# Performance work log

Hardware: AMD Instinct MI355X
Metric: run time of the kernel (lower is better)

## Reference

```python
import jax, jax.numpy as jnp
import numpy as np

D_MODEL = 1024
N_HEADS = 16
D_HEAD = D_MODEL // N_HEADS
LN_EPS = 1e-5


def setup_inputs() -> dict:
    key = jax.random.key(0)
    ks = jax.random.split(key, 6)
    s = 1.0 / np.sqrt(D_MODEL)
    x = jax.random.normal(ks[0], (4, 2048, D_MODEL), dtype=jnp.float32)
    w_qkv = jax.random.uniform(ks[1], (3 * D_MODEL, D_MODEL), jnp.float32, -s, s)
    w_out = jax.random.uniform(ks[2], (D_MODEL, D_MODEL), jnp.float32, -s, s)
    w_ffn1 = jax.random.uniform(ks[3], (2 * D_MODEL, D_MODEL), jnp.float32, -s, s)
    w_ffn2 = jax.random.uniform(ks[4], (D_MODEL, 2 * D_MODEL), jnp.float32, -1.0 / np.sqrt(2 * D_MODEL), 1.0 / np.sqrt(2 * D_MODEL))
    return {
        "x": x,
        "w_qkv": w_qkv,
        "w_out": w_out,
        "w_ffn1": w_ffn1,
        "w_ffn2": w_ffn2,
        "g1": jnp.ones((D_MODEL,), jnp.float32),
        "b1": jnp.zeros((D_MODEL,), jnp.float32),
        "g2": jnp.ones((D_MODEL,), jnp.float32),
        "b2": jnp.zeros((D_MODEL,), jnp.float32),
        "temperature": jnp.float32(0.05),
    }


def _layernorm(x, g, b):
    mu = jnp.mean(x, axis=-1, keepdims=True)
    var = jnp.mean(jnp.square(x - mu), axis=-1, keepdims=True)
    return (x - mu) * jax.lax.rsqrt(var + LN_EPS) * g + b


def _l2norm(x, eps=1e-12):
    # matches F.normalize(p=2, dim=-1)
    n = jnp.sqrt(jnp.sum(jnp.square(x), axis=-1, keepdims=True))
    return x / jnp.maximum(n, eps)


def reference(x, w_qkv, w_out, w_ffn1, w_ffn2, g1, b1, g2, b2, temperature):
    B, N, C = x.shape
    residual = x
    h = _layernorm(x, g1, b1)
    qkv = h @ w_qkv.T  # [B,N,3C]
    qkv = qkv.reshape(B, N, 3, N_HEADS, D_HEAD).transpose(2, 0, 3, 1, 4)
    q, k, v = qkv[0], qkv[1], qkv[2]  # each [B,H,N,d]
    qn = _l2norm(q)
    kn = _l2norm(k)
    attn = jnp.einsum('bhnd,bhmd->bhnm', qn, kn) / temperature
    attn = jax.nn.softmax(attn, axis=-1)
    out = jnp.einsum('bhnm,bhmd->bhnd', attn, v)  # [B,H,N,d]
    out = out.transpose(0, 2, 1, 3).reshape(B, N, C)
    x = residual + out @ w_out.T
    residual = x
    h = _layernorm(x, g2, b2)
    h = jax.nn.relu(h @ w_ffn1.T) @ w_ffn2.T
    return residual + h
```

## Files before the change

### kernel.cpp

```cpp
#include <hip/hip_runtime.h>
#include <cstdint>
#include <cstddef>
#include <math.h>

typedef __attribute__((ext_vector_type(8))) short short8;
typedef __attribute__((ext_vector_type(4))) float f32x4;

#define D_MODEL 1024
#define NHEADS 16
#define DHEAD 64
#define BATCH 4
#define SEQ 2048
#define MTOK (BATCH * SEQ)

__device__ __forceinline__ unsigned short f2bf(float f) {
  union { float f; unsigned u; } v; v.f = f;
  unsigned r = v.u + 0x7fffu + ((v.u >> 16) & 1u);
  return (unsigned short)(r >> 16);
}
__device__ __forceinline__ float bf2f(unsigned short u) {
  union { unsigned u; float f; } v; v.u = ((unsigned)u) << 16;
  return v.f;
}
__device__ __forceinline__ unsigned cvt_pk_bf16(float a, float b) {
  unsigned u;
  asm("v_cvt_pk_bf16_f32 %0, %1, %2" : "=v"(u) : "v"(a), "v"(b));
  return u;
}

typedef const __attribute__((address_space(1))) unsigned int* gas1_t;
typedef __attribute__((address_space(3))) unsigned int* las3_t;
__device__ __forceinline__ void gload16(const unsigned short* g, unsigned short* l) {
  __builtin_amdgcn_global_load_lds((gas1_t)g, (las3_t)l, 16, 0, 0);
}

#define MFMA_BF16(a, b, c) __builtin_amdgcn_mfma_f32_16x16x32_bf16(a, b, c, 0, 0, 0)

__global__ __launch_bounds__(256) void f32_to_bf16_all(const float* __restrict__ s0,
                                                       const float* __restrict__ s1,
                                                       const float* __restrict__ s2,
                                                       const float* __restrict__ s3,
                                                       unsigned short* __restrict__ d0,
                                                       unsigned short* __restrict__ d1,
                                                       unsigned short* __restrict__ d2,
                                                       unsigned short* __restrict__ d3) {
  int j = blockIdx.x * 256 + threadIdx.x;
  const float* s;
  unsigned short* d;
  if (j < 786432) { s = s0; d = d0; }
  else if ((j -= 786432) < 262144) { s = s1; d = d1; }
  else if ((j -= 262144) < 524288) { s = s2; d = d2; }
  else { j -= 524288; s = s3; d = d3; }
  float4 v = ((const float4*)s)[j];
  ushort4 o;
  o.x = f2bf(v.x); o.y = f2bf(v.y); o.z = f2bf(v.z); o.w = f2bf(v.w);
  ((ushort4*)d)[j] = o;
}

__global__ __launch_bounds__(256) void ln_fwd(const float* __restrict__ x, const float* __restrict__ g,
                                              const float* __restrict__ b,
                                              unsigned short* __restrict__ out) {
  const int row = blockIdx.x, t = threadIdx.x;
  float4 v = *(const float4*)(x + (size_t)row * D_MODEL + t * 4);
  float s = v.x + v.y + v.z + v.w;
  float s2 = v.x * v.x + v.y * v.y + v.z * v.z + v.w * v.w;
#pragma unroll
  for (int m = 1; m < 64; m <<= 1) { s += __shfl_xor(s, m); s2 += __shfl_xor(s2, m); }
  __shared__ float red[8];
  int wv = t >> 6;
  if ((t & 63) == 0) { red[wv] = s; red[4 + wv] = s2; }
  __syncthreads();
  s = red[0] + red[1] + red[2] + red[3];
  s2 = red[4] + red[5] + red[6] + red[7];
  float mu = s * (1.f / D_MODEL);
  float var = s2 * (1.f / D_MODEL) - mu * mu;
  float rs = rsqrtf(var + 1e-5f);
  float4 gg = *(const float4*)(g + t * 4);
  float4 bb = *(const float4*)(b + t * 4);
  ushort4 o;
  o.x = f2bf((v.x - mu) * rs * gg.x + bb.x);
  o.y = f2bf((v.y - mu) * rs * gg.y + bb.y);
  o.z = f2bf((v.z - mu) * rs * gg.z + bb.z);
  o.w = f2bf((v.w - mu) * rs * gg.w + bb.w);
  *(ushort4*)(out + (size_t)row * D_MODEL + t * 4) = o;
}

template <int EPI>
__global__ __launch_bounds__(256) void gemm_bt2(const unsigned short* __restrict__ A,
                                                const unsigned short* __restrict__ B,
                                                const float* __restrict__ R,
                                                const float* __restrict__ Tptr,
                                                void* __restrict__ Cout, int M, int N, int K) {
  constexpr int BM = 128, BN = 128, BK = 32;
  __shared__ unsigned short lA[2][BM * BK], lB[2][BN * BK];
  const int tid = threadIdx.x, lane = tid & 63, wave = tid >> 6;
  const int lo = lane & 15, g = lane >> 4;
  const int nbx = gridDim.x;
  const int o = blockIdx.y * nbx + blockIdx.x;
  const int cpx = (nbx * gridDim.y) >> 3;
  const int w = (o & 7) * cpx + (o >> 3);
  const int bx = w % nbx, by = w / nbx;
  const int bm = by * BM, bn = bx * BN;
  const int wr = wave >> 1, wc = wave & 1;
  f32x4 acc[4][4] = {};
  const int c0 = wave * 128 + lane, c1 = c0 + 64;
  const unsigned short* gA0 = A + (size_t)(bm + (c0 >> 2)) * K + (c0 & 3) * 8;
  const unsigned short* gA1 = A + (size_t)(bm + (c1 >> 2)) * K + (c1 & 3) * 8;
  const unsigned short* gB0 = B + (size_t)(bn + (c0 >> 2)) * K + (c0 & 3) * 8;
  const unsigned short* gB1 = B + (size_t)(bn + (c1 >> 2)) * K + (c1 & 3) * 8;
  const int nk = K / BK;
  auto stage = [&](int buf, int kt) {
    const size_t ko = (size_t)kt * BK;
    gload16(gA0 + ko, &lA[buf][(wave * 128) * 8]);
    gload16(gA1 + ko, &lA[buf][(wave * 128 + 64) * 8]);
    gload16(gB0 + ko, &lB[buf][(wave * 128) * 8]);
    gload16(gB1 + ko, &lB[buf][(wave * 128 + 64) * 8]);
  };
  stage(0, 0);
  for (int kt = 0; kt < nk; ++kt) {
    __syncthreads();
    if (kt + 1 < nk) stage((kt + 1) & 1, kt + 1);
    const unsigned short* La = &lA[kt & 1][0];
    const unsigned short* Lb = &lB[kt & 1][0];
    short8 af[4], bfr[4];
#pragma unroll
    for (int m = 0; m < 4; ++m)
      af[m] = *(const short8*)(La + (wr * 64 + m * 16 + lo) * BK + g * 8);
#pragma unroll
    for (int n = 0; n < 4; ++n)
      bfr[n] = *(const short8*)(Lb + (wc * 64 + n * 16 + lo) * BK + g * 8);
#pragma unroll
    for (int m = 0; m < 4; ++m)
#pragma unroll
      for (int n = 0; n < 4; ++n) acc[m][n] = MFMA_BF16(af[m], bfr[n], acc[m][n]);
  }
  const int r0 = bm + wr * 64 + g * 4;
  const int c0c = bn + wc * 64 + lo;
  if (EPI == 3) {
    const int hb = bn + wc * 64;
    const bool isq = hb < 1024, isk = (hb >= 1024) && (hb < 2048);
    const float qs = 1.44269504088896f / Tptr[0];
#pragma unroll
    for (int m = 0; m < 4; ++m)
#pragma unroll
      for (int r = 0; r < 4; ++r) {
        float sc = 1.0f;
        if (isq || isk) {
          float ss = 0.f;
#pragma unroll
          for (int n = 0; n < 4; ++n) ss += acc[m][n][r] * acc[m][n][r];
          ss += __shfl_xor(ss, 1);
          ss += __shfl_xor(ss, 2);
          ss += __shfl_xor(ss, 4);
          ss += __shfl_xor(ss, 8);
          sc = 1.0f / fmaxf(sqrtf(ss), 1e-12f);
          if (isq) sc *= qs;
        }
#pragma unroll
        for (int n = 0; n < 4; ++n) {
          size_t off = (size_t)(r0 + m * 16 + r) * N + (c0c + n * 16);
          ((unsigned short*)Cout)[off] = f2bf(acc[m][n][r] * sc);
        }
      }
  } else {
#pragma unroll
    for (int m = 0; m < 4; ++m)
#pragma unroll
      for (int n = 0; n < 4; ++n) {
#pragma unroll
        for (int r = 0; r < 4; ++r) {
          size_t off = (size_t)(r0 + m * 16 + r) * N + (c0c + n * 16);
          float v = acc[m][n][r];
          if (EPI == 0) ((unsigned short*)Cout)[off] = f2bf(v);
          else if (EPI == 1) ((float*)Cout)[off] = R[off] + v;
          else ((unsigned short*)Cout)[off] = f2bf(fmaxf(v, 0.f));
        }
      }
  }
}

__global__ __launch_bounds__(256) void transpose_v(const unsigned short* __restrict__ qkv,
                                                   unsigned short* __restrict__ vt) {
  __shared__ unsigned short tile[64][80];
  const int blk = blockIdx.x;
  const int ntile = blk & 31, h = (blk >> 5) & 15, b = blk >> 9;
  const int t = threadIdx.x;
  const int tt = t >> 2, c4 = t & 3;
  size_t rowbase = (size_t)(b * SEQ + ntile * 64 + tt) * 3072 + h * 64 + c4 * 16;
  const unsigned short* pv = qkv + rowbase + 2048;
  *(short8*)&tile[tt][c4 * 16] = *(const short8*)pv;
  *(short8*)&tile[tt][c4 * 16 + 8] = *(const short8*)(pv + 8);
  __syncthreads();
  const int d = tt;
  short8 o0, o1;
#pragma unroll
  for (int j = 0; j < 8; ++j) o0[j] = (short)tile[c4 * 16 + j][d];
#pragma unroll
  for (int j = 0; j < 8; ++j) o1[j] = (short)tile[c4 * 16 + 8 + j][d];
  size_t vr = (size_t)((b * NHEADS + h) * DHEAD + d) * SEQ + ntile * 64 + c4 * 16;
  *(short8*)(vt + vr) = o0;
  *(short8*)(vt + vr + 8) = o1;
}

__global__ __launch_bounds__(512) void attn_fwd7(const unsigned short* __restrict__ qkv,
                                                 const unsigned short* __restrict__ vt,
                                                 unsigned short* __restrict__ out,
                                                 const float* __restrict__ temp) {
  constexpr int LDT = 72;
  constexpr int LDP = 66;
  __shared__ unsigned short lK[2][64 * LDT];
  __shared__ unsigned short lV[2][64 * LDT];
  __shared__ unsigned short pP[16][16 * LDP];
  const int d_ = blockIdx.x;
  const int bh = d_ & 63, qt = d_ >> 6;
  const int b = bh >> 4, h = bh & 15;
  const int tid = threadIdx.x, lane = tid & 63, wave = tid >> 6;
  const int lo = lane & 15, g = lane >> 4;
  const int qr0 = qt * 256 + wave * 32;
  const float M0 = 1.05f * 1.44269504088896f / temp[0];
  const f32x4 minit = {-M0, -M0, -M0, -M0};
  const unsigned short* qrowA = qkv + (size_t)(b * SEQ + qr0 + lo) * 3072 + h * 64 + g * 8;
  const unsigned short* qrowB = qrowA + (size_t)16 * 3072;
  const short8 qA0 = *(const short8*)qrowA;
  const short8 qA1 = *(const short8*)(qrowA + 32);
  const short8 qB0 = *(const short8*)qrowB;
  const short8 qB1 = *(const short8*)(qrowB + 32);
  const int srow = tid >> 3, scol = (tid & 7) * 8;
  const unsigned short* gK = qkv + (size_t)(b * SEQ + srow) * 3072 + 1024 + h * 64 + scol;
  const unsigned short* gV = vt + ((size_t)((b * NHEADS + h) * DHEAD) + srow) * SEQ + scol;
  short8 rk = *(const short8*)gK;
  short8 rv = *(const short8*)gV;
  *(short8*)&lK[0][srow * LDT + scol] = rk;
  *(short8*)&lV[0][srow * LDT + scol] = rv;
  f32x4 oA[4] = {}, oB[4] = {};
  float lA_ = 0.f, lB_ = 0.f;
  unsigned short* PbA = &pP[wave][0];
  unsigned short* PbB = &pP[8 + wave][0];
  constexpr int NT = SEQ / 64;
  for (int t = 0; t < NT; ++t) {
    __syncthreads();
    const unsigned short* Kb = &lK[t & 1][0];
    const unsigned short* Vb = &lV[t & 1][0];
    if (t + 1 < NT) {
      rk = *(const short8*)(gK + (size_t)(t + 1) * 64 * 3072);
      rv = *(const short8*)(gV + (t + 1) * 64);
    }
    f32x4 sA[4], sB[4];
    __builtin_amdgcn_s_setprio(1);
#pragma unroll
    for (int jt = 0; jt < 4; ++jt) {
      short8 kf0 = *(const short8*)(Kb + (jt * 16 + lo) * LDT + g * 8);
      short8 kf1 = *(const short8*)(Kb + (jt * 16 + lo) * LDT + 32 + g * 8);
      sA[jt] = MFMA_BF16(kf1, qA1, MFMA_BF16(kf0, qA0, minit));
      sB[jt] = MFMA_BF16(kf1, qB1, MFMA_BF16(kf0, qB0, minit));
    }
    __builtin_amdgcn_s_setprio(0);
    float psA = 0.f, psB = 0.f;
#pragma unroll
    for (int jt = 0; jt < 4; ++jt) {
      float a0 = exp2f(sA[jt][0]), a1 = exp2f(sA[jt][1]);
      float a2 = exp2f(sA[jt][2]), a3 = exp2f(sA[jt][3]);
      sA[jt][0] = a0; sA[jt][1] = a1; sA[jt][2] = a2; sA[jt][3] = a3;
      psA += (a0 + a1) + (a2 + a3);
      float b0 = exp2f(sB[jt][0]), b1 = exp2f(sB[jt][1]);
      float b2 = exp2f(sB[jt][2]), b3 = exp2f(sB[jt][3]);
      sB[jt][0] = b0; sB[jt][1] = b1; sB[jt][2] = b2; sB[jt][3] = b3;
      psB += (b0 + b1) + (b2 + b3);
    }
    lA_ += psA;
    lB_ += psB;
#pragma unroll
    for (int jt = 0; jt < 4; ++jt) {
      *(unsigned*)(PbA + lo * LDP + jt * 16 + g * 4) = cvt_pk_bf16(sA[jt][0], sA[jt][1]);
      *(unsigned*)(PbA + lo * LDP + jt * 16 + g * 4 + 2) = cvt_pk_bf16(sA[jt][2], sA[jt][3]);
      *(unsigned*)(PbB + lo * LDP + jt * 16 + g * 4) = cvt_pk_bf16(sB[jt][0], sB[jt][1]);
      *(unsigned*)(PbB + lo * LDP + jt * 16 + g * 4 + 2) = cvt_pk_bf16(sB[jt][2], sB[jt][3]);
    }
    short8 pA0 = *(const short8*)(PbA + lo * LDP + g * 8);
    short8 pA1 = *(const short8*)(PbA + lo * LDP + 32 + g * 8);
    short8 pB0 = *(const short8*)(PbB + lo * LDP + g * 8);
    short8 pB1 = *(const short8*)(PbB + lo * LDP + 32 + g * 8);
    __builtin_amdgcn_s_setprio(1);
#pragma unroll
    for (int c = 0; c < 4; ++c) {
      short8 vb0 = *(const short8*)(Vb + (c * 16 + lo) * LDT + g * 8);
      short8 vb1 = *(const short8*)(Vb + (c * 16 + lo) * LDT + 32 + g * 8);
      oA[c] = MFMA_BF16(vb1, pA1, MFMA_BF16(vb0, pA0, oA[c]));
      oB[c] = MFMA_BF16(vb1, pB1, MFMA_BF16(vb0, pB0, oB[c]));
    }
    __builtin_amdgcn_s_setprio(0);
    if (t + 1 < NT) {
      *(short8*)&lK[(t + 1) & 1][srow * LDT + scol] = rk;
      *(short8*)&lV[(t + 1) & 1][srow * LDT + scol] = rv;
    }
  }
  lA_ += __shfl_xor(lA_, 16);
  lA_ += __shfl_xor(lA_, 32);
  lB_ += __shfl_xor(lB_, 16);
  lB_ += __shfl_xor(lB_, 32);
  const float rA = 1.0f / lA_, rB = 1.0f / lB_;
  unsigned short* orowA = out + (size_t)(b * SEQ + qr0 + lo) * D_MODEL + h * 64 + g * 4;
  unsigned short* orowB = orowA + (size_t)16 * D_MODEL;
#pragma unroll
  for (int c = 0; c < 4; ++c)
#pragma unroll
    for (int r = 0; r < 4; r += 2) {
      *(unsigned*)(orowA + c * 16 + r) = cvt_pk_bf16(oA[c][r] * rA, oA[c][r + 1] * rA);
      *(unsigned*)(orowB + c * 16 + r) = cvt_pk_bf16(oB[c][r] * rB, oB[c][r + 1] * rB);
    }
}

extern "C" void kernel_launch(void* const* d_in, const int* in_sizes, int n_in, void* d_out,
                              int out_size, void* d_ws, size_t ws_size, hipStream_t stream) {
  const float* x = (const float*)d_in[0];
  const float* w_qkv = (const float*)d_in[1];
  const float* w_out = (const float*)d_in[2];
  const float* w_ffn1 = (const float*)d_in[3];
  const float* w_ffn2 = (const float*)d_in[4];
  const float* g1 = (const float*)d_in[5];
  const float* b1 = (const float*)d_in[6];
  const float* g2 = (const float*)d_in[7];
  const float* b2 = (const float*)d_in[8];
  const float* temp = (const float*)d_in[9];
  float* outp = (float*)d_out;

  char* ws = (char*)d_ws;
  size_t off = 0;
  auto alloc = [&](size_t bytes) {
    void* p = ws + off;
    off += (bytes + 255) & ~(size_t)255;
    return p;
  };
  unsigned short* wqkv_bf = (unsigned short*)alloc((size_t)3072 * 1024 * 2);
  unsigned short* wout_bf = (unsigned short*)alloc((size_t)1024 * 1024 * 2);
  unsigned short* wf1_bf = (unsigned short*)alloc((size_t)2048 * 1024 * 2);
  unsigned short* wf2_bf = (unsigned short*)alloc((size_t)1024 * 2048 * 2);
  unsigned short* h_bf = (unsigned short*)alloc((size_t)MTOK * 1024 * 2);
  unsigned short* qkv_bf = (unsigned short*)alloc((size_t)MTOK * 3072 * 2);
  unsigned short* vt_bf = (unsigned short*)alloc((size_t)BATCH * NHEADS * DHEAD * SEQ * 2);
  unsigned short* ao_bf = (unsigned short*)alloc((size_t)MTOK * 1024 * 2);
  float* x2 = (float*)alloc((size_t)MTOK * 1024 * 4);

  f32_to_bf16_all<<<8192, 256, 0, stream>>>(w_qkv, w_out, w_ffn1, w_ffn2, wqkv_bf, wout_bf, wf1_bf,
                                            wf2_bf);
  ln_fwd<<<MTOK, 256, 0, stream>>>(x, g1, b1, h_bf);
  gemm_bt2<3><<<dim3(3072 / 128, MTOK / 128), 256, 0, stream>>>(h_bf, wqkv_bf, nullptr, temp,
                                                                (void*)qkv_bf, MTOK, 3072, 1024);
  transpose_v<<<BATCH * NHEADS * (SEQ / 64), 256, 0, stream>>>(qkv_bf, vt_bf);
  attn_fwd7<<<BATCH * NHEADS * (SEQ / 256), 512, 0, stream>>>(qkv_bf, vt_bf, ao_bf, temp);
  gemm_bt2<1><<<dim3(1024 / 128, MTOK / 128), 256, 0, stream>>>(ao_bf, wout_bf, x, nullptr,
                                                                (void*)x2, MTOK, 1024, 1024);
  ln_fwd<<<MTOK, 256, 0, stream>>>(x2, g2, b2, h_bf);
  gemm_bt2<2><<<dim3(2048 / 128, MTOK / 128), 256, 0, stream>>>(h_bf, wf1_bf, nullptr, nullptr,
                                                                (void*)qkv_bf, MTOK, 2048, 1024);
  gemm_bt2<1><<<dim3(1024 / 128, MTOK / 128), 256, 0, stream>>>(qkv_bf, wf2_bf, x2, nullptr,
                                                                (void*)outp, MTOK, 1024, 2048);
}
```

Baseline: 367.8 us.

## Rewrite attention with 32x32 MFMA, register P via permlane swap, swizzled LDS

Replaces the 16x16x32 MFMA attention kernel with one built on 32x32x16 MFMA. The softmax probabilities are reshuffled in registers with permlane32_swap, so the LDS round-trip for P goes away. K/V tiles now use an XOR-swizzled unpadded LDS layout instead of padded rows, and blocks shrink to 4 waves covering 128 query rows, which doubles the grid. The aims are fewer LDS accesses and bank conflicts plus denser matrix instructions. The cost is more register pressure and a different occupancy balance.

Result: faster. 347.2 us (-5.6%).

```diff
diff --git a/kernel.cpp b/kernel.cpp
--- a/kernel.cpp
+++ b/kernel.cpp
@@ -5,6 +5,8 @@
 
 typedef __attribute__((ext_vector_type(8))) short short8;
 typedef __attribute__((ext_vector_type(4))) float f32x4;
+typedef __attribute__((ext_vector_type(16))) float f32x16;
+typedef __attribute__((ext_vector_type(2))) unsigned uint2v;
 
 #define D_MODEL 1024
 #define NHEADS 16
@@ -35,6 +37,7 @@
 }
 
 #define MFMA_BF16(a, b, c) __builtin_amdgcn_mfma_f32_16x16x32_bf16(a, b, c, 0, 0, 0)
+#define MFMA32(a, b, c) __builtin_amdgcn_mfma_f32_32x32x16_bf16(a, b, c, 0, 0, 0)
 
 __global__ __launch_bounds__(256) void f32_to_bf16_all(const float* __restrict__ s0,
                                                        const float* __restrict__ s1,
@@ -202,111 +205,113 @@
   *(short8*)(vt + vr + 8) = o1;
 }
 
-__global__ __launch_bounds__(512) void attn_fwd7(const unsigned short* __restrict__ qkv,
+__global__ __launch_bounds__(256) void attn_fwd8(const unsigned short* __restrict__ qkv,
                                                  const unsigned short* __restrict__ vt,
                                                  unsigned short* __restrict__ out,
                                                  const float* __restrict__ temp) {
-  constexpr int LDT = 72;
-  constexpr int LDP = 66;
-  __shared__ unsigned short lK[2][64 * LDT];
-  __shared__ unsigned short lV[2][64 * LDT];
-  __shared__ unsigned short pP[16][16 * LDP];
-  const int d_ = blockIdx.x;
-  const int bh = d_ & 63, qt = d_ >> 6;
+  __shared__ unsigned short lK[2][64 * 64];
+  __shared__ unsigned short lV[2][64 * 64];
+  const int blk = blockIdx.x;
+  const int bh = blk & 63, qt = blk >> 6;
   const int b = bh >> 4, h = bh & 15;
   const int tid = threadIdx.x, lane = tid & 63, wave = tid >> 6;
-  const int lo = lane & 15, g = lane >> 4;
-  const int qr0 = qt * 256 + wave * 32;
+  const int l5 = lane >> 5, l31 = lane & 31;
+  const int qr0 = qt * 128 + wave * 32;
   const float M0 = 1.05f * 1.44269504088896f / temp[0];
-  const f32x4 minit = {-M0, -M0, -M0, -M0};
-  const unsigned short* qrowA = qkv + (size_t)(b * SEQ + qr0 + lo) * 3072 + h * 64 + g * 8;
-  const unsigned short* qrowB = qrowA + (size_t)16 * 3072;
-  const short8 qA0 = *(const short8*)qrowA;
-  const short8 qA1 = *(const short8*)(qrowA + 32);
-  const short8 qB0 = *(const short8*)qrowB;
-  const short8 qB1 = *(const short8*)(qrowB + 32);
-  const int srow = tid >> 3, scol = (tid & 7) * 8;
-  const unsigned short* gK = qkv + (size_t)(b * SEQ + srow) * 3072 + 1024 + h * 64 + scol;
-  const unsigned short* gV = vt + ((size_t)((b * NHEADS + h) * DHEAD) + srow) * SEQ + scol;
-  short8 rk = *(const short8*)gK;
-  short8 rv = *(const short8*)gV;
-  *(short8*)&lK[0][srow * LDT + scol] = rk;
-  *(short8*)&lV[0][srow * LDT + scol] = rv;
-  f32x4 oA[4] = {}, oB[4] = {};
-  float lA_ = 0.f, lB_ = 0.f;
-  unsigned short* PbA = &pP[wave][0];
-  unsigned short* PbB = &pP[8 + wave][0];
+  f32x16 minit;
+#pragma unroll
+  for (int r = 0; r < 16; ++r) minit[r] = -M0;
+  const unsigned short* qrow = qkv + (size_t)(b * SEQ + qr0 + l31) * 3072 + h * 64 + l5 * 8;
+  short8 qf[4];
+#pragma unroll
+  for (int t = 0; t < 4; ++t) qf[t] = *(const short8*)(qrow + t * 16);
+  const int srow = tid >> 3, slot = tid & 7;
+  const int sw0 = ((slot ^ (srow & 7)) * 8);
+  const unsigned short* gK = qkv + (size_t)(b * SEQ + srow) * 3072 + 1024 + h * 64 + slot * 8;
+  const unsigned short* gV = vt + ((size_t)(bh * 64) + srow) * SEQ + slot * 8;
+  short8 rk0 = *(const short8*)gK;
+  short8 rk1 = *(const short8*)(gK + (size_t)32 * 3072);
+  short8 rv0 = *(const short8*)gV;
+  short8 rv1 = *(const short8*)(gV + (size_t)32 * SEQ);
+  *(short8*)&lK[0][srow * 64 + sw0] = rk0;
+  *(short8*)&lK[0][(srow + 32) * 64 + sw0] = rk1;
+  *(short8*)&lV[0][srow * 64 + sw0] = rv0;
+  *(short8*)&lV[0][(srow + 32) * 64 + sw0] = rv1;
+  f32x16 o0 = {}, o1 = {};
+  float lsum = 0.f;
   constexpr int NT = SEQ / 64;
   for (int t = 0; t < NT; ++t) {
     __syncthreads();
     const unsigned short* Kb = &lK[t & 1][0];
     const unsigned short* Vb = &lV[t & 1][0];
     if (t + 1 < NT) {
-      rk = *(const short8*)(gK + (size_t)(t + 1) * 64 * 3072);
-      rv = *(const short8*)(gV + (t + 1) * 64);
+      rk0 = *(const short8*)(gK + (size_t)(t + 1) * 64 * 3072);
+      rk1 = *(const short8*)(gK + (size_t)((t + 1) * 64 + 32) * 3072);
+      rv0 = *(const short8*)(gV + (t + 1) * 64);
+      rv1 = *(const short8*)(gV + (size_t)32 * SEQ + (t + 1) * 64);
     }
-    f32x4 sA[4], sB[4];
-    __builtin_amdgcn_s_setprio(1);
-#pragma unroll
-    for (int jt = 0; jt < 4; ++jt) {
-      short8 kf0 = *(const short8*)(Kb + (jt * 16 + lo) * LDT + g * 8);
-      short8 kf1 = *(const short8*)(Kb + (jt * 16 + lo) * LDT + 32 + g * 8);
-      sA[jt] = MFMA_BF16(kf1, qA1, MFMA_BF16(kf0, qA0, minit));
-      sB[jt] = MFMA_BF16(kf1, qB1, MFMA_BF16(kf0, qB0, minit));
+#pragma unroll
+    for (int tile = 0; tile < 2; ++tile) {
+      f32x16 s = minit;
+      __builtin_amdgcn_s_setprio(1);
+#pragma unroll
+      for (int td = 0; td < 4; ++td) {
+        const int row = tile * 32 + l31;
+        const int sl = ((2 * td + l5) ^ (row & 7)) * 8;
+        short8 kf = *(const short8*)(Kb + row * 64 + sl);
+        s = MFMA32(kf, qf[td], s);
+      }
+      __builtin_amdgcn_s_setprio(0);
+      float p[16];
+      float ps = 0.f;
+#pragma unroll
+      for (int r = 0; r < 16; ++r) { p[r] = exp2f(s[r]); ps += p[r]; }
+      lsum += ps;
+      unsigned a0 = cvt_pk_bf16(p[0], p[1]), a1 = cvt_pk_bf16(p[2], p[3]);
+      unsigned a2 = cvt_pk_bf16(p[4], p[5]), a3 = cvt_pk_bf16(p[6], p[7]);
+      unsigned c0 = cvt_pk_bf16(p[8], p[9]), c1 = cvt_pk_bf16(p[10], p[11]);
+      unsigned c2 = cvt_pk_bf16(p[12], p[13]), c3 = cvt_pk_bf16(p[14], p[15]);
+      uint2v w0 = __builtin_amdgcn_permlane32_swap(a0, a2, false, false);
+      uint2v w1 = __builtin_amdgcn_permlane32_swap(a1, a3, false, false);
+      uint2v w2 = __builtin_amdgcn_permlane32_swap(c0, c2, false, false);
+      uint2v w3 = __builtin_amdgcn_permlane32_swap(c1, c3, false, false);
+      union { unsigned u[4]; short8 v; } f0, f1;
+      f0.u[0] = w0.x; f0.u[1] = w1.x; f0.u[2] = w0.y; f0.u[3] = w1.y;
+      f1.u[0] = w2.x; f1.u[1] = w3.x; f1.u[2] = w2.y; f1.u[3] = w3.y;
+      __builtin_amdgcn_s_setprio(1);
+      {
+        const int vrow0 = l31, vrow1 = 32 + l31;
+        const int sa = ((2 * (tile * 2) + l5) ^ (vrow0 & 7)) * 8;
+        const int sb = ((2 * (tile * 2 + 1) + l5) ^ (vrow0 & 7)) * 8;
+        short8 va0 = *(const short8*)(Vb + vrow0 * 64 + sa);
+        short8 vb0 = *(const short8*)(Vb + vrow0 * 64 + sb);
+        short8 va1 = *(const short8*)(Vb + vrow1 * 64 + sa);
+        short8 vb1 = *(const short8*)(Vb + vrow1 * 64 + sb);
+        o0 = MFMA32(va0, f0.v, o0);
+        o0 = MFMA32(vb0, f1.v, o0);
+        o1 = MFMA32(va1, f0.v, o1);
+        o1 = MFMA32(vb1, f1.v, o1);
+      }
+      __builtin_amdgcn_s_setprio(0);
     }
-    __builtin_amdgcn_s_setprio(0);
-    float psA = 0.f, psB = 0.f;
-#pragma unroll
-    for (int jt = 0; jt < 4; ++jt) {
-      float a0 = exp2f(sA[jt][0]), a1 = exp2f(sA[jt][1]);
-      float a2 = exp2f(sA[jt][2]), a3 = exp2f(sA[jt][3]);
-      sA[jt][0] = a0; sA[jt][1] = a1; sA[jt][2] = a2; sA[jt][3] = a3;
-      psA += (a0 + a1) + (a2 + a3);
-      float b0 = exp2f(sB[jt][0]), b1 = exp2f(sB[jt][1]);
-      float b2 = exp2f(sB[jt][2]), b3 = exp2f(sB[jt][3]);
-      sB[jt][0] = b0; sB[jt][1] = b1; sB[jt][2] = b2; sB[jt][3] = b3;
-      psB += (b0 + b1) + (b2 + b3);
-    }
-    lA_ += psA;
-    lB_ += psB;
-#pragma unroll
-    for (int jt = 0; jt < 4; ++jt) {
-      *(unsigned*)(PbA + lo * LDP + jt * 16 + g * 4) = cvt_pk_bf16(sA[jt][0], sA[jt][1]);
-      *(unsigned*)(PbA + lo * LDP + jt * 16 + g * 4 + 2) = cvt_pk_bf16(sA[jt][2], sA[jt][3]);
-      *(unsigned*)(PbB + lo * LDP + jt * 16 + g * 4) = cvt_pk_bf16(sB[jt][0], sB[jt][1]);
-      *(unsigned*)(PbB + lo * LDP + jt * 16 + g * 4 + 2) = cvt_pk_bf16(sB[jt][2], sB[jt][3]);
-    }
-    short8 pA0 = *(const short8*)(PbA + lo * LDP + g * 8);
-    short8 pA1 = *(const short8*)(PbA + lo * LDP + 32 + g * 8);
-    short8 pB0 = *(const short8*)(PbB + lo * LDP + g * 8);
-    short8 pB1 = *(const short8*)(PbB + lo * LDP + 32 + g * 8);
-    __builtin_amdgcn_s_setprio(1);
-#pragma unroll
-    for (int c = 0; c < 4; ++c) {
-      short8 vb0 = *(const short8*)(Vb + (c * 16 + lo) * LDT + g * 8);
-      short8 vb1 = *(const short8*)(Vb + (c * 16 + lo) * LDT + 32 + g * 8);
-      oA[c] = MFMA_BF16(vb1, pA1, MFMA_BF16(vb0, pA0, oA[c]));
-      oB[c] = MFMA_BF16(vb1, pB1, MFMA_BF16(vb0, pB0, oB[c]));
-    }
-    __builtin_amdgcn_s_setprio(0);
     if (t + 1 < NT) {
-      *(short8*)&lK[(t + 1) & 1][srow * LDT + scol] = rk;
-      *(short8*)&lV[(t + 1) & 1][srow * LDT + scol] = rv;
+      *(short8*)&lK[(t + 1) & 1][srow * 64 + sw0] = rk0;
+      *(short8*)&lK[(t + 1) & 1][(srow + 32) * 64 + sw0] = rk1;
+      *(short8*)&lV[(t + 1) & 1][srow * 64 + sw0] = rv0;
+      *(short8*)&lV[(t + 1) & 1][(srow + 32) * 64 + sw0] = rv1;
     }
   }
-  lA_ += __shfl_xor(lA_, 16);
-  lA_ += __shfl_xor(lA_, 32);
-  lB_ += __shfl_xor(lB_, 16);
-  lB_ += __shfl_xor(lB_, 32);
-  const float rA = 1.0f / lA_, rB = 1.0f / lB_;
-  unsigned short* orowA = out + (size_t)(b * SEQ + qr0 + lo) * D_MODEL + h * 64 + g * 4;
-  unsigned short* orowB = orowA + (size_t)16 * D_MODEL;
-#pragma unroll
-  for (int c = 0; c < 4; ++c)
-#pragma unroll
-    for (int r = 0; r < 4; r += 2) {
-      *(unsigned*)(orowA + c * 16 + r) = cvt_pk_bf16(oA[c][r] * rA, oA[c][r + 1] * rA);
-      *(unsigned*)(orowB + c * 16 + r) = cvt_pk_bf16(oB[c][r] * rB, oB[c][r + 1] * rB);
+  lsum += __shfl_xor(lsum, 32);
+  const float rinv = 1.0f / lsum;
+  unsigned short* orow = out + (size_t)(b * SEQ + qr0 + l31) * D_MODEL + h * 64 + l5 * 4;
+#pragma unroll
+  for (int rq = 0; rq < 4; ++rq)
+#pragma unroll
+    for (int rr = 0; rr < 4; rr += 2) {
+      *(unsigned*)(orow + rq * 8 + rr) =
+          cvt_pk_bf16(o0[rq * 4 + rr] * rinv, o0[rq * 4 + rr + 1] * rinv);
+      *(unsigned*)(orow + 32 + rq * 8 + rr) =
+          cvt_pk_bf16(o1[rq * 4 + rr] * rinv, o1[rq * 4 + rr + 1] * rinv);
     }
 }
 
@@ -347,7 +352,7 @@
   gemm_bt2<3><<<dim3(3072 / 128, MTOK / 128), 256, 0, stream>>>(h_bf, wqkv_bf, nullptr, temp,
                                                                 (void*)qkv_bf, MTOK, 3072, 1024);
   transpose_v<<<BATCH * NHEADS * (SEQ / 64), 256, 0, stream>>>(qkv_bf, vt_bf);
-  attn_fwd7<<<BATCH * NHEADS * (SEQ / 256), 512, 0, stream>>>(qkv_bf, vt_bf, ao_bf, temp);
+  attn_fwd8<<<BATCH * NHEADS * (SEQ / 128), 256, 0, stream>>>(qkv_bf, vt_bf, ao_bf, temp);
   gemm_bt2<1><<<dim3(1024 / 128, MTOK / 128), 256, 0, stream>>>(ao_bf, wout_bf, x, nullptr,
                                                                 (void*)x2, MTOK, 1024, 1024);
   ln_fwd<<<MTOK, 256, 0, stream>>>(x2, g2, b2, h_bf);
```
